# Kernel optimization log

Hardware: AMD Instinct MI355X
Metric: run time of the kernel (lower is better)

## Reference

```python
import jax, jax.numpy as jnp
import numpy as np

GROUPS = 8
EPS = 1e-5


def group_norm(x, gamma, beta):
    # x: [B, C, H, W]; normalize per group over (C/g, H, W)
    B, C, H, W = x.shape
    xg = x.reshape(B, GROUPS, C // GROUPS, H, W)
    mean = xg.mean(axis=(2, 3, 4), keepdims=True)
    var = xg.var(axis=(2, 3, 4), keepdims=True)
    xg = (xg - mean) * jax.lax.rsqrt(var + EPS)
    x = xg.reshape(B, C, H, W)
    return x * gamma[None, :, None, None] + beta[None, :, None, None]


def setup_inputs() -> dict:
    key = jax.random.key(0)
    ks = jax.random.split(key, 6)
    B, C, H, W = 8, 512, 32, 32
    x = jax.random.normal(ks[0], (B, C, H, W), dtype=jnp.float32)
    gn_w = jnp.ones((C,), dtype=jnp.float32)
    gn_b = jnp.zeros((C,), dtype=jnp.float32)
    s = 1.0 / np.sqrt(C)
    qkv_w = jax.random.uniform(ks[1], (3 * C, C), minval=-s, maxval=s, dtype=jnp.float32)
    qkv_b = jax.random.uniform(ks[2], (3 * C,), minval=-s, maxval=s, dtype=jnp.float32)
    proj_w = jax.random.uniform(ks[3], (C, C), minval=-s, maxval=s, dtype=jnp.float32)
    proj_b = jax.random.uniform(ks[4], (C,), minval=-s, maxval=s, dtype=jnp.float32)
    return {"x": x, "gn_w": gn_w, "gn_b": gn_b, "qkv_w": qkv_w,
            "qkv_b": qkv_b, "proj_w": proj_w, "proj_b": proj_b}


def reference(x, gn_w, gn_b, qkv_w, qkv_b, proj_w, proj_b):
    B, C, H, W = x.shape
    xn = group_norm(x, gn_w, gn_b)              # [B,C,H,W] (also the residual)
    xf = xn.reshape(B, C, H * W).transpose(0, 2, 1)  # [B,N,C]
    qkv = jnp.einsum('bnc,dc->bnd', xf, qkv_w) + qkv_b  # [B,N,3C]
    q, k, v = jnp.split(qkv, 3, axis=-1)
    k = jax.nn.softmax(k, axis=-1)              # over channels
    q = jax.nn.softmax(q, axis=-2)              # over tokens
    context = jnp.einsum('bnc,bnd->bcd', k, v)  # [B,C,C]
    out = jnp.einsum('bnc,bcd->bnd', q, context)  # [B,N,C]
    out = jnp.einsum('bnc,dc->bnd', out, proj_w) + proj_b
    out = out.transpose(0, 2, 1).reshape(B, C, H, W)
    return out + xn
```

## Files before the change

### kernel.cpp

```cpp
#include <hip/hip_runtime.h>
#include <hip/hip_bf16.h>
#include <stdint.h>

typedef unsigned short u16;
typedef __attribute__((ext_vector_type(8))) short s16x8;
typedef __attribute__((ext_vector_type(4))) float f32x4;
typedef __attribute__((ext_vector_type(4))) unsigned short u16x4;

static constexpr int B_ = 8, C_ = 512, N_ = 1024, G_ = 8;
static constexpr float EPS = 1e-5f;

static constexpr size_t OFF_XNT  = 0;
static constexpr size_t OFF_Q    = OFF_XNT  + (size_t)B_*N_*C_*2;
static constexpr size_t OFF_K    = OFF_Q    + (size_t)B_*N_*C_*2;
static constexpr size_t OFF_V    = OFF_K    + (size_t)B_*N_*C_*2;
static constexpr size_t OFF_KT   = OFF_V    + (size_t)B_*N_*C_*2;
static constexpr size_t OFF_VT   = OFF_KT   + (size_t)B_*N_*C_*2;
static constexpr size_t OFF_QS   = OFF_VT   + (size_t)B_*N_*C_*2;
static constexpr size_t OFF_CTX  = OFF_QS   + (size_t)B_*N_*C_*2;
static constexpr size_t OFF_MT   = OFF_CTX  + (size_t)B_*C_*C_*2;
static constexpr size_t OFF_WQ   = OFF_MT   + (size_t)B_*C_*C_*2;
static constexpr size_t OFF_WP   = OFF_WQ   + (size_t)3*C_*C_*2;
static constexpr size_t OFF_GNP  = OFF_WP   + (size_t)C_*C_*2;

__device__ __forceinline__ float b2f(u16 u) {
  union { float f; uint32_t i; } x; x.i = ((uint32_t)u) << 16; return x.f;
}
__device__ __forceinline__ u16 f2b(float f) {
  union { float f; uint32_t i; } x; x.f = f;
  return (u16)((x.i + 0x7fffu + ((x.i >> 16) & 1u)) >> 16);
}
#define AS1 __attribute__((address_space(1)))
#define AS3 __attribute__((address_space(3)))
__device__ __forceinline__ void gl2lds16(const void* g, void* l) {
  __builtin_amdgcn_global_load_lds((const AS1 void*)g, (AS3 void*)l, 16, 0, 0);
}

__global__ __launch_bounds__(256) void pre_kernel(const float* __restrict__ x,
                                                  float* __restrict__ gnp,
                                                  const float* __restrict__ w1,
                                                  const float* __restrict__ w2,
                                                  u16* __restrict__ o1,
                                                  u16* __restrict__ o2) {
  int bid = blockIdx.x;
  if (bid < 512) {
    int bg = bid >> 3, chunk = bid & 7;
    const float4* p = reinterpret_cast<const float4*>(x + (size_t)bg * 65536 + (size_t)chunk * 8192);
    int tid = threadIdx.x;
    float s = 0.f, sq = 0.f;
#pragma unroll
    for (int i = 0; i < 8; ++i) {
      float4 v = p[i * 256 + tid];
      s  += v.x + v.y + v.z + v.w;
      sq += v.x*v.x + v.y*v.y + v.z*v.z + v.w*v.w;
    }
    for (int off = 32; off; off >>= 1) { s += __shfl_xor(s, off); sq += __shfl_xor(sq, off); }
    __shared__ float red[8];
    int wid = tid >> 6, lane = tid & 63;
    if (lane == 0) { red[wid*2] = s; red[wid*2+1] = sq; }
    __syncthreads();
    if (tid == 0) {
      gnp[(bg*8 + chunk)*2 + 0] = red[0]+red[2]+red[4]+red[6];
      gnp[(bg*8 + chunk)*2 + 1] = red[1]+red[3]+red[5]+red[7];
    }
  } else {
    int i = (bid - 512) * 256 + threadIdx.x;
    const int n1 = 1536*512/4;
    if (i < n1) {
      float4 v = reinterpret_cast<const float4*>(w1)[i];
      u16x4 r = { f2b(v.x), f2b(v.y), f2b(v.z), f2b(v.w) };
      reinterpret_cast<u16x4*>(o1)[i] = r;
    } else {
      int j = i - n1;
      float4 v = reinterpret_cast<const float4*>(w2)[j];
      u16x4 r = { f2b(v.x), f2b(v.y), f2b(v.z), f2b(v.w) };
      reinterpret_cast<u16x4*>(o2)[j] = r;
    }
  }
}

__global__ __launch_bounds__(256) void gn_apply(const float* __restrict__ x,
                                                const float* __restrict__ gw,
                                                const float* __restrict__ gb,
                                                const float* __restrict__ gnp,
                                                u16* __restrict__ xnT) {
  __shared__ float T[64][65];
  int b = blockIdx.x, c0 = blockIdx.y * 64, n0 = blockIdx.z * 64;
  int bg = b * G_ + blockIdx.y;
  float S = 0.f, SQ = 0.f;
#pragma unroll
  for (int i = 0; i < 8; ++i) { S += gnp[(bg*8+i)*2]; SQ += gnp[(bg*8+i)*2+1]; }
  float mean = S * (1.f/65536.f);
  float var  = SQ * (1.f/65536.f) - mean*mean;
  float rstd = rsqrtf(var + EPS);
  int tn = threadIdx.x & 63, tc = threadIdx.x >> 6;
#pragma unroll 4
  for (int it = 0; it < 16; ++it) {
    int cl = it*4 + tc;
    int c = c0 + cl;
    float v = x[((size_t)b*C_ + c)*N_ + n0 + tn];
    T[tn][cl] = (v - mean) * rstd * gw[c] + gb[c];
  }
  __syncthreads();
#pragma unroll
  for (int p = 0; p < 2; ++p) {
    int nl = p*32 + (threadIdx.x >> 3);
    int cs = (threadIdx.x & 7) * 8;
    s16x8 o;
#pragma unroll
    for (int j = 0; j < 8; ++j) o[j] = (short)f2b(T[nl][cs + j]);
    *reinterpret_cast<s16x8*>(&xnT[((size_t)(b*N_ + n0 + nl))*C_ + c0 + cs]) = o;
  }
}

__global__ __launch_bounds__(512, 2) void gemm_qkv8(const u16* __restrict__ A,
                                                    const u16* __restrict__ Bm,
                                                    const float* __restrict__ bias,
                                                    u16* __restrict__ Oq,
                                                    u16* __restrict__ Ok,
                                                    u16* __restrict__ Ov) {
  const int lda = 512, ldb = 512;
  __shared__ u16 As[2][256*64];
  __shared__ u16 Bs[2][256*64];
  int tid = threadIdx.x, wid = tid >> 6, lane = tid & 63;
  int wr = wid >> 2, wc = wid & 3;
  int m0 = blockIdx.x * 256, n0 = blockIdx.y * 256;

  f32x4 acc[8][4] = {};
  int sr = lane >> 3;
  int sg = (lane & 7) ^ sr;

  auto stage = [&](int buf, int k0) {
#pragma unroll
    for (int t = 0; t < 4; ++t) {
      int chunk = wid*4 + t;
      gl2lds16(A  + (size_t)(m0 + chunk*8 + sr)*lda + k0 + sg*8,
               (void*)(&As[buf][chunk*512]));
      gl2lds16(Bm + (size_t)(n0 + chunk*8 + sr)*ldb + k0 + sg*8,
               (void*)(&Bs[buf][chunk*512]));
    }
  };

  stage(0, 0);
  int cur = 0;
  for (int kt = 0; kt < 8; ++kt) {
    if (kt + 1 < 8) {
      stage(cur ^ 1, (kt + 1) * 64);
      asm volatile("s_waitcnt vmcnt(8)" ::: "memory");
    } else {
      asm volatile("s_waitcnt vmcnt(0)" ::: "memory");
    }
    __builtin_amdgcn_s_barrier();
    __builtin_amdgcn_sched_barrier(0);

#pragma unroll
    for (int q = 0; q < 4; ++q) {
      const int qa = q >> 1, qb = q & 1;
      s16x8 af[4][2], bfq[2][2];
#pragma unroll
      for (int mi2 = 0; mi2 < 4; ++mi2)
#pragma unroll
        for (int ks2 = 0; ks2 < 2; ++ks2) {
          int ar = wr*128 + qa*64 + mi2*16 + (lane & 15);
          int s  = ks2*4 + (lane >> 4);
          af[mi2][ks2] = *reinterpret_cast<const s16x8*>(&As[cur][ar*64 + ((s ^ (ar & 7)) << 3)]);
        }
#pragma unroll
      for (int ni2 = 0; ni2 < 2; ++ni2)
#pragma unroll
        for (int ks2 = 0; ks2 < 2; ++ks2) {
          int br = wc*64 + qb*32 + ni2*16 + (lane & 15);
          int s  = ks2*4 + (lane >> 4);
          bfq[ni2][ks2] = *reinterpret_cast<const s16x8*>(&Bs[cur][br*64 + ((s ^ (br & 7)) << 3)]);
        }
      __builtin_amdgcn_s_setprio(1);
#pragma unroll
      for (int mi2 = 0; mi2 < 4; ++mi2)
#pragma unroll
        for (int ni2 = 0; ni2 < 2; ++ni2)
#pragma unroll
          for (int ks2 = 0; ks2 < 2; ++ks2)
            acc[qa*4 + mi2][qb*2 + ni2] =
              __builtin_amdgcn_mfma_f32_16x16x32_bf16(af[mi2][ks2], bfq[ni2][ks2],
                                                      acc[qa*4 + mi2][qb*2 + ni2], 0, 0, 0);
      __builtin_amdgcn_s_setprio(0);
    }

    asm volatile("s_waitcnt lgkmcnt(0)" ::: "memory");
    __builtin_amdgcn_s_barrier();
    __builtin_amdgcn_sched_barrier(0);
    cur ^= 1;
  }

  u16* Odst; int cbase;
  if (n0 < 512)       { Odst = Oq; cbase = n0; }
  else if (n0 < 1024) { Odst = Ok; cbase = n0 - 512; }
  else                { Odst = Ov; cbase = n0 - 1024; }
#pragma unroll
  for (int mi = 0; mi < 8; ++mi) {
#pragma unroll
    for (int ni = 0; ni < 4; ++ni) {
      int cseg = cbase + wc*64 + ni*16 + (lane & 15);
      float bi = bias[n0 + wc*64 + ni*16 + (lane & 15)];
#pragma unroll
      for (int r = 0; r < 4; ++r) {
        int row = m0 + wr*128 + mi*16 + (lane >> 4)*4 + r;
        Odst[(size_t)row*512 + cseg] = f2b(acc[mi][ni][r] + bi);
      }
    }
  }
}

template<int BM, int BN, int EPI>
__global__ __launch_bounds__(256) void gemm(const u16* __restrict__ A,
                                            const u16* __restrict__ Bm,
                                            int M, int N, int K, int lda, int ldb,
                                            long strideA, long strideB, long strideC,
                                            const float* __restrict__ bias,
                                            void* __restrict__ O0,
                                            const void* __restrict__ R) {
  constexpr int BK = 64;
  constexpr int MI = BM / 32, NI = BN / 32;
  __shared__ u16 As[2][BM*BK];
  __shared__ u16 Bs[2][BN*BK];
  int tid = threadIdx.x, wid = tid >> 6, lane = tid & 63;
  int m0 = blockIdx.x * BM, n0 = blockIdx.y * BN;
  const u16* Ab = A + (size_t)strideA * blockIdx.z;
  const u16* Bp = Bm + (size_t)strideB * blockIdx.z;

  f32x4 acc[MI][NI] = {};
  int wm = (wid >> 1) * (BM/2), wn = (wid & 1) * (BN/2);
  int sr = lane >> 3;
  int sg = (lane & 7) ^ sr;

  auto stage = [&](int buf, int k0) {
#pragma unroll
    for (int t = 0; t < BM/32; ++t) {
      int chunk = wid*(BM/32) + t;
      gl2lds16(Ab + (size_t)(m0 + chunk*8 + sr)*lda + k0 + sg*8,
               (void*)(&As[buf][chunk*512]));
    }
#pragma unroll
    for (int t = 0; t < BN/32; ++t) {
      int chunk = wid*(BN/32) + t;
      gl2lds16(Bp + (size_t)(n0 + chunk*8 + sr)*ldb + k0 + sg*8,
               (void*)(&Bs[buf][chunk*512]));
    }
  };

  int KT = K / BK;
  stage(0, 0);
  __syncthreads();
  int cur = 0;
  for (int kt = 0; kt < KT; ++kt) {
    if (kt + 1 < KT) stage(cur ^ 1, (kt + 1) * BK);
#pragma unroll
    for (int ks = 0; ks < BK; ks += 32) {
      int s = (ks >> 3) + (lane >> 4);
      s16x8 af[MI], bfr[NI];
#pragma unroll
      for (int mi = 0; mi < MI; ++mi) {
        int ar = wm + mi*16 + (lane & 15);
        af[mi] = *reinterpret_cast<const s16x8*>(&As[cur][ar*64 + ((s ^ (ar & 7)) << 3)]);
      }
#pragma unroll
      for (int ni = 0; ni < NI; ++ni) {
        int br = wn + ni*16 + (lane & 15);
        bfr[ni] = *reinterpret_cast<const s16x8*>(&Bs[cur][br*64 + ((s ^ (br & 7)) << 3)]);
      }
#pragma unroll
      for (int mi = 0; mi < MI; ++mi)
#pragma unroll
        for (int ni = 0; ni < NI; ++ni)
          acc[mi][ni] = __builtin_amdgcn_mfma_f32_16x16x32_bf16(af[mi], bfr[ni], acc[mi][ni], 0, 0, 0);
    }
    __syncthreads();
    cur ^= 1;
  }

#pragma unroll
  for (int mi = 0; mi < MI; ++mi) {
#pragma unroll
    for (int ni = 0; ni < NI; ++ni) {
      int col = n0 + wn + ni*16 + (lane & 15);
      if constexpr (EPI == 2) {
        int n = m0 + wm + mi*16 + (lane >> 4)*4;
        int b = blockIdx.z;
        const u16* xr = (const u16*)R + ((size_t)(b*N_ + n))*C_ + col;
        size_t idx = (size_t)b*524288 + (size_t)col*1024 + n;
        float bi = bias[col];
        float4 o;
        o.x = acc[mi][ni][0] + bi + b2f(xr[0]);
        o.y = acc[mi][ni][1] + bi + b2f(xr[512]);
        o.z = acc[mi][ni][2] + bi + b2f(xr[1024]);
        o.w = acc[mi][ni][3] + bi + b2f(xr[1536]);
        *reinterpret_cast<float4*>((float*)O0 + idx) = o;
      } else {
#pragma unroll
        for (int r = 0; r < 4; ++r) {
          int row = m0 + wm + mi*16 + (lane >> 4)*4 + r;
          ((u16*)O0)[(size_t)strideC*blockIdx.z + (size_t)row*N + col] = f2b(acc[mi][ni][r]);
        }
      }
    }
  }
}

__global__ __launch_bounds__(256) void mid_kernel(const u16* __restrict__ kin,
                                                  const u16* __restrict__ vin,
                                                  u16* __restrict__ kT,
                                                  u16* __restrict__ vT,
                                                  const u16* __restrict__ q,
                                                  u16* __restrict__ qs) {
  __shared__ __align__(16) char smem[33024];
  int bid = blockIdx.x;
  if (bid < 256) {
    u16 (*T)[516] = (u16(*)[516])smem;
    int b = bid >> 5, n0 = (bid & 31) * 32;
    int wid = threadIdx.x >> 6, lane = threadIdx.x & 63;

#pragma unroll
    for (int i = 0; i < 8; ++i) {
      int r = wid * 8 + i;
      const u16* p = kin + ((size_t)(b*N_ + n0 + r))*C_;
      s16x8 raw = reinterpret_cast<const s16x8*>(p)[lane];
      float v[8]; float m = -3e38f;
#pragma unroll
      for (int j = 0; j < 8; ++j) { v[j] = b2f((u16)raw[j]); m = fmaxf(m, v[j]); }
      for (int off = 32; off; off >>= 1) m = fmaxf(m, __shfl_xor(m, off));
      float s = 0.f;
#pragma unroll
      for (int j = 0; j < 8; ++j) { v[j] = __expf(v[j] - m); s += v[j]; }
      for (int off = 32; off; off >>= 1) s += __shfl_xor(s, off);
      float inv = 1.f / s;
      union { s16x8 v8; unsigned long long d[2]; } o;
#pragma unroll
      for (int j = 0; j < 8; ++j) o.v8[j] = (short)f2b(v[j] * inv);
      unsigned long long* dst = reinterpret_cast<unsigned long long*>(&T[r][lane*8]);
      dst[0] = o.d[0]; dst[1] = o.d[1];
    }
    __syncthreads();
#pragma unroll
    for (int h = 0; h < 2; ++h) {
      int c = h*256 + threadIdx.x;
      u16* dst = kT + ((size_t)(b*C_ + c))*N_ + n0;
#pragma unroll
      for (int q4 = 0; q4 < 4; ++q4) {
        s16x8 o;
#pragma unroll
        for (int j = 0; j < 8; ++j) o[j] = (short)T[q4*8 + j][c];
        reinterpret_cast<s16x8*>(dst)[q4] = o;
      }
    }
    __syncthreads();

#pragma unroll
    for (int i = 0; i < 8; ++i) {
      int r = wid * 8 + i;
      const u16* p = vin + ((size_t)(b*N_ + n0 + r))*C_;
      union { s16x8 v8; unsigned long long d[2]; } o;
      o.v8 = reinterpret_cast<const s16x8*>(p)[lane];
      unsigned long long* dst = reinterpret_cast<unsigned long long*>(&T[r][lane*8]);
      dst[0] = o.d[0]; dst[1] = o.d[1];
    }
    __syncthreads();
#pragma unroll
    for (int h = 0; h < 2; ++h) {
      int c = h*256 + threadIdx.x;
      u16* dst = vT + ((size_t)(b*C_ + c))*N_ + n0;
#pragma unroll
      for (int q4 = 0; q4 < 4; ++q4) {
        s16x8 o;
#pragma unroll
        for (int j = 0; j < 8; ++j) o[j] = (short)T[q4*8 + j][c];
        reinterpret_cast<s16x8*>(dst)[q4] = o;
      }
    }
  } else {
    float (*Mr)[65] = (float(*)[65])smem;
    float (*Sr)[65] = (float(*)[65])(smem + 8320);
    float (*MS)[2]  = (float(*)[2]) (smem + 16640);
    int j2 = bid - 256;
    int b = j2 >> 4, c0 = (j2 & 15) * 32;
    int t = threadIdx.x;
    int cg = t & 3;
    int rw = t >> 2;
    const u16* base = q + (size_t)b*N_*C_ + c0 + cg*8;
    float m[8], s[8];
#pragma unroll
    for (int j = 0; j < 8; ++j) { m[j] = -3e38f; s[j] = 0.f; }
    for (int it = 0; it < 16; ++it) {
      int n = it*64 + rw;
      s16x8 raw = *reinterpret_cast<const s16x8*>(base + (size_t)n*C_);
#pragma unroll
      for (int j = 0; j < 8; ++j) {
        float v = b2f((u16)raw[j]);
        float nm = fmaxf(m[j], v);
        s[j] = s[j]*__expf(m[j] - nm) + __expf(v - nm);
        m[j] = nm;
      }
    }
#pragma unroll
    for (int j = 0; j < 8; ++j) { Mr[cg*8 + j][rw] = m[j]; Sr[cg*8 + j][rw] = s[j]; }
    __syncthreads();
    if (t < 32) {
      float M = -3e38f;
      for (int i = 0; i < 64; ++i) M = fmaxf(M, Mr[t][i]);
      float S = 0.f;
      for (int i = 0; i < 64; ++i) S += Sr[t][i]*__expf(Mr[t][i] - M);
      MS[t][0] = M; MS[t][1] = 1.f / S;
    }
    __syncthreads();
    float Mv[8], Iv[8];
#pragma unroll
    for (int j = 0; j < 8; ++j) { Mv[j] = MS[cg*8 + j][0]; Iv[j] = MS[cg*8 + j][1]; }
    u16* ob = qs + (size_t)b*N_*C_ + c0 + cg*8;
    for (int it = 0; it < 16; ++it) {
      int n = it*64 + rw;
      s16x8 raw = *reinterpret_cast<const s16x8*>(base + (size_t)n*C_);
      s16x8 o;
#pragma unroll
      for (int j = 0; j < 8; ++j)
        o[j] = (short)f2b(__expf(b2f((u16)raw[j]) - Mv[j]) * Iv[j]);
      *reinterpret_cast<s16x8*>(ob + (size_t)n*C_) = o;
    }
  }
}

extern "C" void kernel_launch(void* const* d_in, const int* in_sizes, int n_in,
                              void* d_out, int out_size, void* d_ws, size_t ws_size,
                              hipStream_t stream) {
  (void)in_sizes; (void)n_in; (void)out_size; (void)ws_size;
  const float* x      = (const float*)d_in[0];
  const float* gn_w   = (const float*)d_in[1];
  const float* gn_b   = (const float*)d_in[2];
  const float* qkv_w  = (const float*)d_in[3];
  const float* qkv_b  = (const float*)d_in[4];
  const float* proj_w = (const float*)d_in[5];
  const float* proj_b = (const float*)d_in[6];

  char* ws = (char*)d_ws;
  u16*   xnT  = (u16*)  (ws + OFF_XNT);
  u16*   qb   = (u16*)  (ws + OFF_Q);
  u16*   kb   = (u16*)  (ws + OFF_K);
  u16*   vb   = (u16*)  (ws + OFF_V);
  u16*   kT   = (u16*)  (ws + OFF_KT);
  u16*   vT   = (u16*)  (ws + OFF_VT);
  u16*   qsb  = (u16*)  (ws + OFF_QS);
  u16*   ctx  = (u16*)  (ws + OFF_CTX);
  u16*   mt   = (u16*)  (ws + OFF_MT);
  u16*   wq   = (u16*)  (ws + OFF_WQ);
  u16*   wp   = (u16*)  (ws + OFF_WP);
  float* gnp  = (float*)(ws + OFF_GNP);

  pre_kernel<<<dim3(1536), 256, 0, stream>>>(x, gnp, qkv_w, proj_w, wq, wp);
  gn_apply<<<dim3(8, 8, 16), 256, 0, stream>>>(x, gn_w, gn_b, gnp, xnT);

  gemm_qkv8<<<dim3(32, 6), 512, 0, stream>>>(xnT, wq, qkv_b, qb, kb, vb);

  mid_kernel<<<dim3(384), 256, 0, stream>>>(kb, vb, kT, vT, qb, qsb);

  gemm<64,64,1><<<dim3(8, 8, 8), 256, 0, stream>>>(kT, vT, 512, 512, 1024, 1024, 1024,
                                                   524288, 524288, 262144, nullptr, ctx, nullptr);
  gemm<64,64,1><<<dim3(8, 8, 8), 256, 0, stream>>>(wp, ctx, 512, 512, 512, 512, 512,
                                                   0, 262144, 262144, nullptr, mt, nullptr);
  gemm<64,64,2><<<dim3(16, 8, 8), 256, 0, stream>>>(qsb, mt, 1024, 512, 512, 512, 512,
                                                    524288, 262144, 0, proj_b, (float*)d_out, xnT);
}
```

Before: 163.1 us.

## Write V transposed directly from QKV GEMM epilogue via LDS staging

The QKV GEMM blocks that produce V now transpose their tile through shared memory and write V^T directly. This removes the separate V buffer and the V transpose pass in mid_kernel, saving an 8 MB write plus its read-back. The GEMM main loop is also restructured: B fragments are loaded once per k-step rather than per quadrant, and the hand-placed waitcnt/sched barriers are replaced with plain __syncthreads. That may reduce the load/compute overlap and add register pressure.

```diff
diff --git a/kernel.cpp b/kernel.cpp
--- a/kernel.cpp
+++ b/kernel.cpp
@@ -13,8 +13,7 @@
 static constexpr size_t OFF_XNT  = 0;
 static constexpr size_t OFF_Q    = OFF_XNT  + (size_t)B_*N_*C_*2;
 static constexpr size_t OFF_K    = OFF_Q    + (size_t)B_*N_*C_*2;
-static constexpr size_t OFF_V    = OFF_K    + (size_t)B_*N_*C_*2;
-static constexpr size_t OFF_KT   = OFF_V    + (size_t)B_*N_*C_*2;
+static constexpr size_t OFF_KT   = OFF_K    + (size_t)B_*N_*C_*2;
 static constexpr size_t OFF_VT   = OFF_KT   + (size_t)B_*N_*C_*2;
 static constexpr size_t OFF_QS   = OFF_VT   + (size_t)B_*N_*C_*2;
 static constexpr size_t OFF_CTX  = OFF_QS   + (size_t)B_*N_*C_*2;
@@ -118,10 +117,9 @@
                                                     const float* __restrict__ bias,
                                                     u16* __restrict__ Oq,
                                                     u16* __restrict__ Ok,
-                                                    u16* __restrict__ Ov) {
+                                                    u16* __restrict__ OvT) {
   const int lda = 512, ldb = 512;
-  __shared__ u16 As[2][256*64];
-  __shared__ u16 Bs[2][256*64];
+  __shared__ u16 smem[4][16384];
   int tid = threadIdx.x, wid = tid >> 6, lane = tid & 63;
   int wr = wid >> 2, wc = wid & 3;
   int m0 = blockIdx.x * 256, n0 = blockIdx.y * 256;
@@ -135,77 +133,102 @@
     for (int t = 0; t < 4; ++t) {
       int chunk = wid*4 + t;
       gl2lds16(A  + (size_t)(m0 + chunk*8 + sr)*lda + k0 + sg*8,
-               (void*)(&As[buf][chunk*512]));
+               (void*)(&smem[0 + buf][chunk*512]));
       gl2lds16(Bm + (size_t)(n0 + chunk*8 + sr)*ldb + k0 + sg*8,
-               (void*)(&Bs[buf][chunk*512]));
+               (void*)(&smem[2 + buf][chunk*512]));
     }
   };
 
   stage(0, 0);
+  __syncthreads();
   int cur = 0;
   for (int kt = 0; kt < 8; ++kt) {
-    if (kt + 1 < 8) {
-      stage(cur ^ 1, (kt + 1) * 64);
-      asm volatile("s_waitcnt vmcnt(8)" ::: "memory");
-    } else {
-      asm volatile("s_waitcnt vmcnt(0)" ::: "memory");
-    }
-    __builtin_amdgcn_s_barrier();
-    __builtin_amdgcn_sched_barrier(0);
-
-#pragma unroll
-    for (int q = 0; q < 4; ++q) {
-      const int qa = q >> 1, qb = q & 1;
-      s16x8 af[4][2], bfq[2][2];
+    if (kt + 1 < 8) stage(cur ^ 1, (kt + 1) * 64);
+
+    s16x8 bfr[4][2];
+#pragma unroll
+    for (int ni = 0; ni < 4; ++ni)
+#pragma unroll
+      for (int ks2 = 0; ks2 < 2; ++ks2) {
+        int br = wc*64 + ni*16 + (lane & 15);
+        int s  = ks2*4 + (lane >> 4);
+        bfr[ni][ks2] = *reinterpret_cast<const s16x8*>(&smem[2 + cur][br*64 + ((s ^ (br & 7)) << 3)]);
+      }
+#pragma unroll
+    for (int qa = 0; qa < 2; ++qa) {
+      s16x8 af[4][2];
 #pragma unroll
       for (int mi2 = 0; mi2 < 4; ++mi2)
 #pragma unroll
         for (int ks2 = 0; ks2 < 2; ++ks2) {
           int ar = wr*128 + qa*64 + mi2*16 + (lane & 15);
           int s  = ks2*4 + (lane >> 4);
-          af[mi2][ks2] = *reinterpret_cast<const s16x8*>(&As[cur][ar*64 + ((s ^ (ar & 7)) << 3)]);
-        }
-#pragma unroll
-      for (int ni2 = 0; ni2 < 2; ++ni2)
-#pragma unroll
-        for (int ks2 = 0; ks2 < 2; ++ks2) {
-          int br = wc*64 + qb*32 + ni2*16 + (lane & 15);
-          int s  = ks2*4 + (lane >> 4);
-          bfq[ni2][ks2] = *reinterpret_cast<const s16x8*>(&Bs[cur][br*64 + ((s ^ (br & 7)) << 3)]);
+          af[mi2][ks2] = *reinterpret_cast<const s16x8*>(&smem[0 + cur][ar*64 + ((s ^ (ar & 7)) << 3)]);
         }
       __builtin_amdgcn_s_setprio(1);
 #pragma unroll
       for (int mi2 = 0; mi2 < 4; ++mi2)
 #pragma unroll
-        for (int ni2 = 0; ni2 < 2; ++ni2)
+        for (int ni = 0; ni < 4; ++ni)
 #pragma unroll
           for (int ks2 = 0; ks2 < 2; ++ks2)
-            acc[qa*4 + mi2][qb*2 + ni2] =
-              __builtin_amdgcn_mfma_f32_16x16x32_bf16(af[mi2][ks2], bfq[ni2][ks2],
-                                                      acc[qa*4 + mi2][qb*2 + ni2], 0, 0, 0);
+            acc[qa*4 + mi2][ni] =
+              __builtin_amdgcn_mfma_f32_16x16x32_bf16(af[mi2][ks2], bfr[ni][ks2],
+                                                      acc[qa*4 + mi2][ni], 0, 0, 0);
       __builtin_amdgcn_s_setprio(0);
     }
 
-    asm volatile("s_waitcnt lgkmcnt(0)" ::: "memory");
-    __builtin_amdgcn_s_barrier();
-    __builtin_amdgcn_sched_barrier(0);
+    __syncthreads();
     cur ^= 1;
   }
 
-  u16* Odst; int cbase;
-  if (n0 < 512)       { Odst = Oq; cbase = n0; }
-  else if (n0 < 1024) { Odst = Ok; cbase = n0 - 512; }
-  else                { Odst = Ov; cbase = n0 - 1024; }
-#pragma unroll
-  for (int mi = 0; mi < 8; ++mi) {
-#pragma unroll
-    for (int ni = 0; ni < 4; ++ni) {
-      int cseg = cbase + wc*64 + ni*16 + (lane & 15);
-      float bi = bias[n0 + wc*64 + ni*16 + (lane & 15)];
-#pragma unroll
-      for (int r = 0; r < 4; ++r) {
-        int row = m0 + wr*128 + mi*16 + (lane >> 4)*4 + r;
-        Odst[(size_t)row*512 + cseg] = f2b(acc[mi][ni][r] + bi);
+  if (n0 < 1024) {
+    u16* Odst; int cbase;
+    if (n0 < 512) { Odst = Oq; cbase = n0; }
+    else          { Odst = Ok; cbase = n0 - 512; }
+#pragma unroll
+    for (int mi = 0; mi < 8; ++mi) {
+#pragma unroll
+      for (int ni = 0; ni < 4; ++ni) {
+        int cseg = cbase + wc*64 + ni*16 + (lane & 15);
+        float bi = bias[n0 + wc*64 + ni*16 + (lane & 15)];
+#pragma unroll
+        for (int r = 0; r < 4; ++r) {
+          int row = m0 + wr*128 + mi*16 + (lane >> 4)*4 + r;
+          Odst[(size_t)row*512 + cseg] = f2b(acc[mi][ni][r] + bi);
+        }
+      }
+    }
+  } else {
+    int cb = n0 - 1024;
+    int bidx = m0 >> 10;
+    int npart = m0 & 1023;
+    u16 (*T)[136] = reinterpret_cast<u16(*)[136]>(&smem[0][0]);
+#pragma unroll
+    for (int h = 0; h < 2; ++h) {
+      __syncthreads();
+      if (wr == h) {
+#pragma unroll
+        for (int mi = 0; mi < 8; ++mi)
+#pragma unroll
+          for (int ni = 0; ni < 4; ++ni) {
+            int d = wc*64 + ni*16 + (lane & 15);
+            float bi = bias[1024 + cb + d];
+#pragma unroll
+            for (int r = 0; r < 4; ++r) {
+              int trow = mi*16 + (lane >> 4)*4 + r;
+              T[d][trow] = f2b(acc[mi][ni][r] + bi);
+            }
+          }
+      }
+      __syncthreads();
+#pragma unroll
+      for (int i = 0; i < 8; ++i) {
+        int idx2 = tid + 512*i;
+        int d  = idx2 >> 4;
+        int ns = idx2 & 15;
+        s16x8 vseg = *reinterpret_cast<const s16x8*>(&T[d][ns*8]);
+        *reinterpret_cast<s16x8*>(&OvT[((size_t)(bidx*512 + cb + d))*1024 + npart + h*128 + ns*8]) = vseg;
       }
     }
   }
@@ -307,9 +330,7 @@
 }
 
 __global__ __launch_bounds__(256) void mid_kernel(const u16* __restrict__ kin,
-                                                  const u16* __restrict__ vin,
                                                   u16* __restrict__ kT,
-                                                  u16* __restrict__ vT,
                                                   const u16* __restrict__ q,
                                                   u16* __restrict__ qs) {
   __shared__ __align__(16) char smem[33024];
@@ -318,7 +339,6 @@
     u16 (*T)[516] = (u16(*)[516])smem;
     int b = bid >> 5, n0 = (bid & 31) * 32;
     int wid = threadIdx.x >> 6, lane = threadIdx.x & 63;
-
 #pragma unroll
     for (int i = 0; i < 8; ++i) {
       int r = wid * 8 + i;
@@ -344,30 +364,6 @@
     for (int h = 0; h < 2; ++h) {
       int c = h*256 + threadIdx.x;
       u16* dst = kT + ((size_t)(b*C_ + c))*N_ + n0;
-#pragma unroll
-      for (int q4 = 0; q4 < 4; ++q4) {
-        s16x8 o;
-#pragma unroll
-        for (int j = 0; j < 8; ++j) o[j] = (short)T[q4*8 + j][c];
-        reinterpret_cast<s16x8*>(dst)[q4] = o;
-      }
-    }
-    __syncthreads();
-
-#pragma unroll
-    for (int i = 0; i < 8; ++i) {
-      int r = wid * 8 + i;
-      const u16* p = vin + ((size_t)(b*N_ + n0 + r))*C_;
-      union { s16x8 v8; unsigned long long d[2]; } o;
-      o.v8 = reinterpret_cast<const s16x8*>(p)[lane];
-      unsigned long long* dst = reinterpret_cast<unsigned long long*>(&T[r][lane*8]);
-      dst[0] = o.d[0]; dst[1] = o.d[1];
-    }
-    __syncthreads();
-#pragma unroll
-    for (int h = 0; h < 2; ++h) {
-      int c = h*256 + threadIdx.x;
-      u16* dst = vT + ((size_t)(b*C_ + c))*N_ + n0;
 #pragma unroll
       for (int q4 = 0; q4 < 4; ++q4) {
         s16x8 o;
@@ -443,7 +439,6 @@
   u16*   xnT  = (u16*)  (ws + OFF_XNT);
   u16*   qb   = (u16*)  (ws + OFF_Q);
   u16*   kb   = (u16*)  (ws + OFF_K);
-  u16*   vb   = (u16*)  (ws + OFF_V);
   u16*   kT   = (u16*)  (ws + OFF_KT);
   u16*   vT   = (u16*)  (ws + OFF_VT);
   u16*   qsb  = (u16*)  (ws + OFF_QS);
@@ -456,9 +451,9 @@
   pre_kernel<<<dim3(1536), 256, 0, stream>>>(x, gnp, qkv_w, proj_w, wq, wp);
   gn_apply<<<dim3(8, 8, 16), 256, 0, stream>>>(x, gn_w, gn_b, gnp, xnT);
 
-  gemm_qkv8<<<dim3(32, 6), 512, 0, stream>>>(xnT, wq, qkv_b, qb, kb, vb);
-
-  mid_kernel<<<dim3(384), 256, 0, stream>>>(kb, vb, kT, vT, qb, qsb);
+  gemm_qkv8<<<dim3(32, 6), 512, 0, stream>>>(xnT, wq, qkv_b, qb, kb, vT);
+
+  mid_kernel<<<dim3(384), 256, 0, stream>>>(kb, kT, qb, qsb);
 
   gemm<64,64,1><<<dim3(8, 8, 8), 256, 0, stream>>>(kT, vT, 512, 512, 1024, 1024, 1024,
                                                    524288, 524288, 262144, nullptr, ctx, nullptr);
```

Result: faster. 155.1 us (-4.9%).
